# Kernel optimization log

Measured on AMD Instinct MI355X. Metric: run time of the kernel, lower is better.

## Reference

```python
import jax, jax.numpy as jnp
import numpy as np

B, T, D = 2, 2048, 1024
H, DH, CTX = 16, 64, 2048
EPS = 1e-6

def setup_inputs() -> dict:
    key = jax.random.key(0)
    ks = jax.random.split(key, 8)
    s = lambda d: 1.0 / np.sqrt(d)
    return {
        'x':       jax.random.normal(ks[0], (B, T, D), jnp.float32),
        'w_norm1': jnp.ones((D,), jnp.float32),
        'w_qkv':   jax.random.normal(ks[1], (3 * D, D), jnp.float32) * s(D),
        'w_proj':  jax.random.normal(ks[2], (D, D), jnp.float32) * s(D),
        'w_norm2': jnp.ones((D,), jnp.float32),
        'w_gate':  jax.random.normal(ks[3], (4 * D, D), jnp.float32) * s(D),
        'w_up':    jax.random.normal(ks[4], (4 * D, D), jnp.float32) * s(D),
        'w_down':  jax.random.normal(ks[5], (D, 4 * D), jnp.float32) * s(4 * D),
        'step':    0,
    }

def _rmsnorm(x, w):
    return x * jax.lax.rsqrt(jnp.mean(x * x, axis=-1, keepdims=True) + EPS) * w

def reference(x, w_norm1, w_qkv, w_proj, w_norm2, w_gate, w_up, w_down, step):
    # Prefill path (kv_cache is None, step == 0): full causal attention over T tokens.
    b, t, d = x.shape
    scale = 1.0 / np.sqrt(DH)
    h = _rmsnorm(x, w_norm1)
    qkv = (h @ w_qkv.T).reshape(b, t, 3, H, DH).transpose(2, 0, 3, 1, 4)  # [3,B,H,T,Dh]
    q, k, v = qkv[0], qkv[1], qkv[2]
    att = jnp.einsum('bhqd,bhkd->bhqk', q, k) * scale           # [B,H,T,T]
    causal = jnp.tril(jnp.ones((t, t), bool))
    att = jnp.where(causal, att, jnp.float32(-jnp.inf))
    att = jax.nn.softmax(att, axis=-1)
    out = jnp.einsum('bhqk,bhkd->bhqd', att, v)                 # [B,H,T,Dh]
    out = out.transpose(0, 2, 1, 3).reshape(b, t, d)
    x = x + out @ w_proj.T
    h2 = _rmsnorm(x, w_norm2)
    x = x + (jax.nn.silu(h2 @ w_gate.T) * (h2 @ w_up.T)) @ w_down.T
    # Append-only KV cache, zero-padded to ctx length as in the torch module.
    k_cache = jnp.zeros((b, H, CTX, DH), x.dtype).at[:, :, :t].set(k)
    v_cache = jnp.zeros((b, H, CTX, DH), x.dtype).at[:, :, :t].set(v)
    return (x, k_cache, v_cache)
```

## Files before the change

kernel.cpp:

```cpp
#include <hip/hip_runtime.h>
#include <hip/hip_bf16.h>
#include <cstdint>
#include <cstddef>


using bf16x8 = __attribute__((ext_vector_type(8))) __bf16;
using f32x4  = __attribute__((ext_vector_type(4))) float;

#define VMCNT(n) asm volatile("s_waitcnt vmcnt(" #n ")" ::: "memory")
#define LGKM0()  do { asm volatile("s_waitcnt lgkmcnt(0)" ::: "memory"); \
                      __builtin_amdgcn_sched_barrier(0); } while (0)
#define BARF()   do { asm volatile("" ::: "memory"); __builtin_amdgcn_s_barrier(); \
                      asm volatile("" ::: "memory"); } while (0)

__device__ __forceinline__ short f2b(float f) {
  uint32_t u = __builtin_bit_cast(uint32_t, f);
  uint32_t r = (u + 0x7FFFu + ((u >> 16) & 1u)) >> 16;
  return (short)r;
}
__device__ __forceinline__ float b2f(short s) {
  uint32_t u = ((uint32_t)(uint16_t)s) << 16;
  return __builtin_bit_cast(float, u);
}
__device__ __forceinline__ uint32_t pack2(float a, float b) {
  return (__builtin_bit_cast(uint32_t, a) >> 16) |
         (__builtin_bit_cast(uint32_t, b) & 0xFFFF0000u);
}

__device__ __forceinline__ void gload16(const short* g, short* l) {
  __builtin_amdgcn_global_load_lds(
      (const __attribute__((address_space(1))) void*)g,
      (__attribute__((address_space(3))) void*)l, 16, 0, 0);
}

template<int ROWS>
__device__ __forceinline__ void stage_swz(const short* __restrict__ g, int ldg,
                                          short* lds, int tid) {
#pragma unroll
  for (int jj = 0; jj < ROWS / 32; ++jj) {
    int row = jj * 32 + (tid >> 3);
    int seg = tid & 7;
    gload16(g + (size_t)row * ldg + ((seg ^ (row & 7)) << 3),
            lds + row * 64 + (seg << 3));
  }
}

__device__ __forceinline__ void stage_round512(const short* __restrict__ g, int ldg,
                                               short* lds, int tid, int rbase) {
  int row = rbase + (tid >> 3);
  int seg = tid & 7;
  gload16(g + (size_t)row * ldg + ((seg ^ (row & 7)) << 3),
          lds + row * 64 + (seg << 3));
}

__device__ __forceinline__ bf16x8 frag64(const short* lds, int row, int seg) {
  return *(const bf16x8*)(lds + row * 64 + ((seg ^ (row & 7)) << 3));
}

__device__ __forceinline__ f32x4 mma16(bf16x8 a, bf16x8 b, f32x4 c) {
  return __builtin_amdgcn_mfma_f32_16x16x32_bf16(a, b, c, 0, 0, 0);
}

__global__ void k_cvt_all(const float* __restrict__ wqkv, short* __restrict__ oqkv,
                          const float* __restrict__ wproj, short* __restrict__ oproj,
                          const float* __restrict__ wgate, short* __restrict__ ogate,
                          const float* __restrict__ wup, short* __restrict__ oup,
                          const float* __restrict__ wdown, short* __restrict__ odown) {
  int bid = blockIdx.x;
  const float* src;
  short* dst;
  int off;
  if (bid < 3072)       { src = wqkv;  dst = oqkv;  off = bid; }
  else if (bid < 4096)  { src = wproj; dst = oproj; off = bid - 3072; }
  else if (bid < 8192)  { src = wgate; dst = ogate; off = bid - 4096; }
  else if (bid < 12288) { src = wup;   dst = oup;   off = bid - 8192; }
  else                  { src = wdown; dst = odown; off = bid - 12288; }
  int i = off * 256 + threadIdx.x;
  float4 v = ((const float4*)src)[i];
  ((short4*)dst)[i] = make_short4(f2b(v.x), f2b(v.y), f2b(v.z), f2b(v.w));
}

__global__ void k_rms(const float* __restrict__ x, const float* __restrict__ w,
                      short* __restrict__ out) {
  int row = blockIdx.x;
  int tid = threadIdx.x;
  float4 v = *(const float4*)(x + (size_t)row * 1024 + tid * 4);
  float ss = v.x * v.x + v.y * v.y + v.z * v.z + v.w * v.w;
#pragma unroll
  for (int o = 1; o < 64; o <<= 1) ss += __shfl_xor(ss, o);
  __shared__ float sred[4];
  int wid = tid >> 6, lane = tid & 63;
  if (lane == 0) sred[wid] = ss;
  __syncthreads();
  float tot = sred[0] + sred[1] + sred[2] + sred[3];
  float r = rsqrtf(tot * (1.0f / 1024.0f) + 1e-6f);
  float4 wv = *(const float4*)(w + tid * 4);
  short4 o = make_short4(f2b(v.x * r * wv.x), f2b(v.y * r * wv.y),
                         f2b(v.z * r * wv.z), f2b(v.w * r * wv.w));
  *(short4*)(out + (size_t)row * 1024 + tid * 4) = o;
}

template<int MODE>
__global__ __launch_bounds__(512, 2) void k_gemm_big(
    const short* __restrict__ A, const short* __restrict__ Bw,
    int M, int N, int K, int gx,
    short* __restrict__ outb,
    short* __restrict__ q_b, short* __restrict__ k_b, short* __restrict__ vT_b,
    float* __restrict__ kc, float* __restrict__ vc) {
  __shared__ short As[2][256 * 64];
  __shared__ short Bs[2][256 * 64];
  int tid = threadIdx.x;
  int nwg = gridDim.x, bid = blockIdx.x;
  int swz = (bid & 7) * (nwg >> 3) + (bid >> 3);
  int bx = swz % gx, by = swz / gx;
  int m0 = by * 256, n0 = bx * 256;
  int w = tid >> 6, l = tid & 63;
  int wr = w >> 2, wc = w & 3;
  int lr = l & 15, lseg = l >> 4;
  f32x4 acc[2][2][4][2] = {};
  int nk = K >> 6;
  const short* Ab = A + (size_t)m0 * K;
  const short* Bb = Bw + (size_t)n0 * K;

  stage_round512(Ab, K, &As[0][0], tid, 0);
  stage_round512(Ab, K, &As[0][0], tid, 64);
  stage_round512(Ab, K, &As[0][0], tid, 128);
  stage_round512(Ab, K, &As[0][0], tid, 192);
  stage_round512(Bb, K, &Bs[0][0], tid, 0);
  stage_round512(Bb, K, &Bs[0][0], tid, 64);
  stage_round512(Bb, K, &Bs[0][0], tid, 128);
  stage_round512(Bb, K, &Bs[0][0], tid, 192);
  stage_round512(Ab + 64, K, &As[1][0], tid, 0);
  stage_round512(Ab + 64, K, &As[1][0], tid, 128);
  stage_round512(Ab + 64, K, &As[1][0], tid, 64);
  stage_round512(Ab + 64, K, &As[1][0], tid, 192);
  stage_round512(Bb + 64, K, &Bs[1][0], tid, 0);
  stage_round512(Bb + 64, K, &Bs[1][0], tid, 64);

  bf16x8 a0[4][2], a1[4][2], bq[2][2];
#pragma unroll 2
  for (int t = 0; t < nk; ++t) {
    short* Sa  = &As[t & 1][0];
    short* Sb  = &Bs[t & 1][0];
    short* Sb1 = &Bs[(t + 1) & 1][0];
    const short* Ag2 = Ab + (size_t)(t + 2) * 64;
    const short* Bg1 = Bb + (size_t)(t + 1) * 64;
    const short* Bg2 = Bb + (size_t)(t + 2) * 64;
    bool pf1 = (t + 1 < nk), pf2 = (t + 2 < nk);

    VMCNT(6);
    BARF();

#pragma unroll
    for (int i = 0; i < 4; ++i)
#pragma unroll
      for (int kk = 0; kk < 2; ++kk)
        a0[i][kk] = frag64(Sa, wr * 128 + i * 16 + lr, kk * 4 + lseg);
#pragma unroll
    for (int j = 0; j < 2; ++j)
#pragma unroll
      for (int kk = 0; kk < 2; ++kk)
        bq[j][kk] = frag64(Sb, wc * 64 + j * 16 + lr, kk * 4 + lseg);
    if (pf1) {
      stage_round512(Bg1, K, Sb1, tid, 128);
      stage_round512(Bg1, K, Sb1, tid, 192);
    }
    BARF();
    LGKM0();
    __builtin_amdgcn_s_setprio(1);
#pragma unroll
    for (int i = 0; i < 4; ++i)
#pragma unroll
      for (int j = 0; j < 2; ++j) {
        acc[0][0][i][j] = mma16(a0[i][0], bq[j][0], acc[0][0][i][j]);
        acc[0][0][i][j] = mma16(a0[i][1], bq[j][1], acc[0][0][i][j]);
      }
    __builtin_amdgcn_s_setprio(0);

#pragma unroll
    for (int i = 0; i < 4; ++i)
#pragma unroll
      for (int kk = 0; kk < 2; ++kk)
        a1[i][kk] = frag64(Sa, wr * 128 + 64 + i * 16 + lr, kk * 4 + lseg);
    if (pf2) {
      stage_round512(Ag2, K, Sa, tid, 0);
      stage_round512(Ag2, K, Sa, tid, 128);
    }
    BARF();
    LGKM0();
    __builtin_amdgcn_s_setprio(1);
#pragma unroll
    for (int i = 0; i < 4; ++i)
#pragma unroll
      for (int j = 0; j < 2; ++j) {
        acc[1][0][i][j] = mma16(a1[i][0], bq[j][0], acc[1][0][i][j]);
        acc[1][0][i][j] = mma16(a1[i][1], bq[j][1], acc[1][0][i][j]);
      }
    __builtin_amdgcn_s_setprio(0);

#pragma unroll
    for (int j = 0; j < 2; ++j)
#pragma unroll
      for (int kk = 0; kk < 2; ++kk)
        bq[j][kk] = frag64(Sb, wc * 64 + 32 + j * 16 + lr, kk * 4 + lseg);
    if (pf2) {
      stage_round512(Ag2, K, Sa, tid, 64);
      stage_round512(Ag2, K, Sa, tid, 192);
    }
    BARF();
    LGKM0();
    __builtin_amdgcn_s_setprio(1);
#pragma unroll
    for (int i = 0; i < 4; ++i)
#pragma unroll
      for (int j = 0; j < 2; ++j) {
        acc[0][1][i][j] = mma16(a0[i][0], bq[j][0], acc[0][1][i][j]);
        acc[0][1][i][j] = mma16(a0[i][1], bq[j][1], acc[0][1][i][j]);
      }
    __builtin_amdgcn_s_setprio(0);

    if (pf2) {
      stage_round512(Bg2, K, Sb, tid, 0);
      stage_round512(Bg2, K, Sb, tid, 64);
    }
    BARF();
    __builtin_amdgcn_s_setprio(1);
#pragma unroll
    for (int i = 0; i < 4; ++i)
#pragma unroll
      for (int j = 0; j < 2; ++j) {
        acc[1][1][i][j] = mma16(a1[i][0], bq[j][0], acc[1][1][i][j]);
        acc[1][1][i][j] = mma16(a1[i][1], bq[j][1], acc[1][1][i][j]);
      }
    __builtin_amdgcn_s_setprio(0);
  }

#pragma unroll
  for (int qm = 0; qm < 2; ++qm) {
#pragma unroll
    for (int qn = 0; qn < 2; ++qn) {
#pragma unroll
      for (int i = 0; i < 4; ++i) {
#pragma unroll
        for (int j = 0; j < 2; ++j) {
#pragma unroll
          for (int r = 0; r < 4; ++r) {
            int m = m0 + wr * 128 + qm * 64 + i * 16 + (l >> 4) * 4 + r;
            int n = n0 + wc * 64 + qn * 32 + j * 16 + lr;
            float f = acc[qm][qn][i][j][r];
            if (MODE == 1) {
              outb[(size_t)m * N + n] = f2b(f);
            } else if (MODE == 2) {
              float g = b2f(outb[(size_t)m * N + n]);
              float sg = g / (1.0f + __expf(-g));
              outb[(size_t)m * N + n] = f2b(sg * f);
            } else {
              int jj = n >> 10, hh = (n >> 6) & 15, dh = n & 63;
              int b_ = m >> 11, t = m & 2047;
              int bhh = b_ * 16 + hh;
              size_t idx = ((size_t)bhh * 2048 + t) * 64 + dh;
              if (jj == 0) {
                q_b[idx] = f2b(f);
              } else if (jj == 1) {
                k_b[idx] = f2b(f);
                kc[idx] = f;
              } else {
                vT_b[((size_t)bhh * 64 + dh) * 2048 + t] = f2b(f);
                vc[idx] = f;
              }
            }
          }
        }
      }
    }
  }
}

__global__ __launch_bounds__(256, 2) void k_gemm_skinny(
    const short* __restrict__ A, const short* __restrict__ Bw,
    int M, int N, int K, int gx,
    const float* __restrict__ res, float* __restrict__ outf) {
  __shared__ short As[3][128 * 64];
  __shared__ short Bs[3][64 * 64];
  int tid = threadIdx.x;
  int nwg = gridDim.x, bid = blockIdx.x;
  int swz = (bid & 7) * (nwg >> 3) + (bid >> 3);
  int bx = swz % gx, by = swz / gx;
  int m0 = by * 128, n0 = bx * 64;
  int w = tid >> 6, l = tid & 63;
  int wr = w >> 1, wc = w & 1;
  int lr = l & 15, lseg = l >> 4;
  f32x4 acc[4][2] = {};
  int nk = K >> 6;
  const short* Ab = A + (size_t)m0 * K;
  const short* Bb = Bw + (size_t)n0 * K;

  stage_swz<128>(Ab, K, &As[0][0], tid);
  stage_swz<64>(Bb, K, &Bs[0][0], tid);
  stage_swz<128>(Ab + 64, K, &As[1][0], tid);
  stage_swz<64>(Bb + 64, K, &Bs[1][0], tid);

#pragma unroll 1
  for (int u = 0; u < nk; ++u) {
    VMCNT(6);
    BARF();
    if (u + 2 < nk) {
      int sl = (u + 2) % 3;
      stage_swz<128>(Ab + (u + 2) * 64, K, &As[sl][0], tid);
      stage_swz<64>(Bb + (u + 2) * 64, K, &Bs[sl][0], tid);
    }
    const short* Asl = &As[u % 3][0];
    const short* Bsl = &Bs[u % 3][0];
    bf16x8 ar[4][2], br[2][2];
#pragma unroll
    for (int i = 0; i < 4; ++i)
#pragma unroll
      for (int kk = 0; kk < 2; ++kk)
        ar[i][kk] = frag64(Asl, wr * 64 + i * 16 + lr, kk * 4 + lseg);
#pragma unroll
    for (int j = 0; j < 2; ++j)
#pragma unroll
      for (int kk = 0; kk < 2; ++kk)
        br[j][kk] = frag64(Bsl, wc * 32 + j * 16 + lr, kk * 4 + lseg);
    LGKM0();
    __builtin_amdgcn_s_setprio(1);
#pragma unroll
    for (int i = 0; i < 4; ++i)
#pragma unroll
      for (int j = 0; j < 2; ++j) {
        acc[i][j] = mma16(ar[i][0], br[j][0], acc[i][j]);
        acc[i][j] = mma16(ar[i][1], br[j][1], acc[i][j]);
      }
    __builtin_amdgcn_s_setprio(0);
  }

#pragma unroll
  for (int i = 0; i < 4; ++i) {
#pragma unroll
    for (int j = 0; j < 2; ++j) {
#pragma unroll
      for (int r = 0; r < 4; ++r) {
        int m = m0 + wr * 64 + i * 16 + (l >> 4) * 4 + r;
        int n = n0 + wc * 32 + j * 16 + lr;
        outf[(size_t)m * N + n] = acc[i][j][r] + res[(size_t)m * N + n];
      }
    }
  }
}

template<int NC>
__device__ __forceinline__ void attn_tile(
    const short* __restrict__ Ksl, const short* __restrict__ Vsl,
    short* __restrict__ pw,
    const bf16x8 (&qf)[2][2], f32x4 (&acc)[2][4],
    float (&mrow)[2], float (&dden)[2],
    int kv0, int qb0, int qb1, bool band0, bool band1,
    int lr, int g) {
  bf16x8 kf[4][2], vb[2][4];
#pragma unroll
  for (int i = 0; i < 4; ++i)
#pragma unroll
    for (int kk = 0; kk < 2; ++kk)
      kf[i][kk] = frag64(Ksl, i * 16 + lr, kk * 4 + g);
#pragma unroll
  for (int kk = 0; kk < 2; ++kk)
#pragma unroll
    for (int jf = 0; jf < 4; ++jf)
      vb[kk][jf] = frag64(Vsl, jf * 16 + lr, kk * 4 + g);

  f32x4 st[NC][4];
#pragma unroll
  for (int c = 0; c < NC; ++c) {
    int cc = (NC == 2) ? c : 1;
#pragma unroll
    for (int i = 0; i < 4; ++i) {
      f32x4 z = {};
      z = mma16(kf[i][0], qf[cc][0], z);
      z = mma16(kf[i][1], qf[cc][1], z);
      st[c][i] = z;
    }
  }

  const float SC = 0.125f * 1.44269504f;
  float p[NC][16], pm[NC], corr[NC];
#pragma unroll
  for (int c = 0; c < NC; ++c) {
    int cc = (NC == 2) ? c : 1;
    bool band = (cc == 0) ? band0 : band1;
    int qgc = ((cc == 0) ? qb0 : qb1) + lr;
    float m_ = -INFINITY;
#pragma unroll
    for (int i = 0; i < 4; ++i)
#pragma unroll
      for (int r = 0; r < 4; ++r) {
        float v = st[c][i][r] * SC;
        if (band) {
          int key = kv0 + i * 16 + g * 4 + r;
          if (key > qgc) v = -INFINITY;
        }
        p[c][i * 4 + r] = v;
        m_ = fmaxf(m_, v);
      }
    pm[c] = m_;
  }
#pragma unroll
  for (int c = 0; c < NC; ++c) pm[c] = fmaxf(pm[c], __shfl_xor(pm[c], 16));
#pragma unroll
  for (int c = 0; c < NC; ++c) pm[c] = fmaxf(pm[c], __shfl_xor(pm[c], 32));
  float dsum[NC];
#pragma unroll
  for (int c = 0; c < NC; ++c) {
    int cc = (NC == 2) ? c : 1;
    float nm = fmaxf(mrow[cc], pm[c]);
    corr[c] = exp2f(mrow[cc] - nm);
    mrow[cc] = nm;
    float ds_ = 0.0f;
#pragma unroll
    for (int kx = 0; kx < 16; ++kx) {
      float pv = exp2f(p[c][kx] - nm);
      p[c][kx] = pv;
      ds_ += pv;
    }
    dsum[c] = ds_;
  }
#pragma unroll
  for (int c = 0; c < NC; ++c) dsum[c] += __shfl_xor(dsum[c], 16);
#pragma unroll
  for (int c = 0; c < NC; ++c) dsum[c] += __shfl_xor(dsum[c], 32);
#pragma unroll
  for (int c = 0; c < NC; ++c) {
    int cc = (NC == 2) ? c : 1;
    dden[cc] = dden[cc] * corr[c] + dsum[c];
  }

#pragma unroll
  for (int c = 0; c < NC; ++c) {
    int cc = (NC == 2) ? c : 1;
#pragma unroll
    for (int r = 0; r < 4; ++r) {
      float cr = __shfl(corr[c], g * 4 + r);
#pragma unroll
      for (int jf = 0; jf < 4; ++jf) acc[cc][jf][r] *= cr;
    }
    int prow = cc * 16 + lr;
#pragma unroll
    for (int i = 0; i < 4; ++i) {
      uint2 pk;
      pk.x = pack2(p[c][i * 4 + 0], p[c][i * 4 + 1]);
      pk.y = pack2(p[c][i * 4 + 2], p[c][i * 4 + 3]);
      int seg = (i * 2 + (g >> 1)) ^ (prow & 7);
      *(uint2*)(pw + prow * 64 + seg * 8 + (g & 1) * 4) = pk;
    }
  }

#pragma unroll
  for (int c = 0; c < NC; ++c) {
    int cc = (NC == 2) ? c : 1;
    int prow = cc * 16 + lr;
#pragma unroll
    for (int kk = 0; kk < 2; ++kk) {
      bf16x8 pa = *(const bf16x8*)(pw + prow * 64 + (((kk * 4 + g) ^ (prow & 7)) << 3));
#pragma unroll
      for (int jf = 0; jf < 4; ++jf)
        acc[cc][jf] = mma16(pa, vb[kk][jf], acc[cc][jf]);
    }
  }
}

__global__ __launch_bounds__(256, 2) void k_attn(const short* __restrict__ q_b,
                                                 const short* __restrict__ k_b,
                                                 const short* __restrict__ vT_b,
                                                 short* __restrict__ o_b) {
  __shared__ short Ks[3][64 * 64];
  __shared__ short VTs[3][64 * 64];
  __shared__ short Ps[4][32 * 64];
  int tid = threadIdx.x;
  int w = tid >> 6, l = tid & 63;
  int lr = l & 15, g = l >> 4;
  int ib = blockIdx.x, bh = blockIdx.y;
  int qlo = ib, qhi = 31 - ib;
  int qb0 = qlo * 64 + w * 16;
  int qb1 = qhi * 64 + w * 16;

  bf16x8 qf[2][2];
  const short* Qg = q_b + (size_t)bh * 2048 * 64;
#pragma unroll
  for (int kk = 0; kk < 2; ++kk) {
    qf[0][kk] = *(const bf16x8*)(Qg + (size_t)(qb0 + lr) * 64 + kk * 32 + g * 8);
    qf[1][kk] = *(const bf16x8*)(Qg + (size_t)(qb1 + lr) * 64 + kk * 32 + g * 8);
  }

  f32x4 acc[2][4] = {};
  float mrow[2] = {-INFINITY, -INFINITY};
  float dden[2] = {0.0f, 0.0f};
  int nt = qhi + 1;
  const short* Kg = k_b + (size_t)bh * 2048 * 64;
  const short* Vg = vT_b + (size_t)bh * 64 * 2048;
  short* pw = &Ps[w][0];

  stage_swz<64>(Kg, 64, &Ks[0][0], tid);
  stage_swz<64>(Vg, 2048, &VTs[0][0], tid);
  stage_swz<64>(Kg + 64 * 64, 64, &Ks[1][0], tid);
  stage_swz<64>(Vg + 64, 2048, &VTs[1][0], tid);

#pragma unroll 1
  for (int kt = 0; kt <= qlo; ++kt) {
    VMCNT(4);
    BARF();
    if (kt + 2 < nt) {
      int sl = (kt + 2) % 3;
      stage_swz<64>(Kg + (size_t)(kt + 2) * 64 * 64, 64, &Ks[sl][0], tid);
      stage_swz<64>(Vg + (kt + 2) * 64, 2048, &VTs[sl][0], tid);
    }
    int s = kt % 3;
    attn_tile<2>(&Ks[s][0], &VTs[s][0], pw, qf, acc, mrow, dden,
                 kt * 64, qb0, qb1, kt == qlo, false, lr, g);
  }
#pragma unroll 1
  for (int kt = qlo + 1; kt < nt; ++kt) {
    VMCNT(4);
    BARF();
    if (kt + 2 < nt) {
      int sl = (kt + 2) % 3;
      stage_swz<64>(Kg + (size_t)(kt + 2) * 64 * 64, 64, &Ks[sl][0], tid);
      stage_swz<64>(Vg + (kt + 2) * 64, 2048, &VTs[sl][0], tid);
    }
    int s = kt % 3;
    attn_tile<1>(&Ks[s][0], &VTs[s][0], pw, qf, acc, mrow, dden,
                 kt * 64, qb0, qb1, false, kt == qhi, lr, g);
  }

  int hh = bh & 15, b_ = bh >> 4;
#pragma unroll
  for (int c = 0; c < 2; ++c) {
    int qbc = (c == 0) ? qb0 : qb1;
#pragma unroll
    for (int r = 0; r < 4; ++r) {
      float dq = __shfl(dden[c], g * 4 + r);
      float inv = 1.0f / dq;
      int mg = qbc + g * 4 + r;
      size_t rowoff = ((size_t)b_ * 2048 + mg) * 1024 + hh * 64;
#pragma unroll
      for (int jf = 0; jf < 4; ++jf)
        o_b[rowoff + jf * 16 + lr] = f2b(acc[c][jf][r] * inv);
    }
  }
}

extern "C" void kernel_launch(void* const* d_in, const int* in_sizes, int n_in,
                              void* d_out, int out_size, void* d_ws, size_t ws_size,
                              hipStream_t stream) {
  const float* x     = (const float*)d_in[0];
  const float* wn1   = (const float*)d_in[1];
  const float* wqkv  = (const float*)d_in[2];
  const float* wproj = (const float*)d_in[3];
  const float* wn2   = (const float*)d_in[4];
  const float* wgate = (const float*)d_in[5];
  const float* wup   = (const float*)d_in[6];
  const float* wdown = (const float*)d_in[7];
  float* out = (float*)d_out;
  char* ws = (char*)d_ws;

  short* wqkv_b  = (short*)(ws + 0);
  short* wproj_b = (short*)(ws + 6291456);
  short* wgate_b = (short*)(ws + 8388608);
  short* wup_b   = (short*)(ws + 16777216);
  short* wdown_b = (short*)(ws + 25165824);
  short* h_b     = (short*)(ws + 33554432);
  short* q_b     = (short*)(ws + 41943040);
  short* k_b     = (short*)(ws + 50331648);
  short* vT_b    = (short*)(ws + 58720256);
  short* ao_b    = (short*)(ws + 67108864);
  short* act_b   = q_b;
  float* x1 = out;
  float* kc = out + 4194304;
  float* vc = out + 8388608;

  k_cvt_all<<<16384, 256, 0, stream>>>(wqkv, wqkv_b, wproj, wproj_b,
                                       wgate, wgate_b, wup, wup_b, wdown, wdown_b);

  k_rms<<<4096, 256, 0, stream>>>(x, wn1, h_b);

  k_gemm_big<3><<<192, 512, 0, stream>>>(h_b, wqkv_b, 4096, 3072, 1024, 12,
                                         nullptr, q_b, k_b, vT_b, kc, vc);

  k_attn<<<dim3(16, 32), 256, 0, stream>>>(q_b, k_b, vT_b, ao_b);

  k_gemm_skinny<<<512, 256, 0, stream>>>(ao_b, wproj_b, 4096, 1024, 1024, 16,
                                         x, x1);

  k_rms<<<4096, 256, 0, stream>>>(x1, wn2, h_b);

  k_gemm_big<1><<<256, 512, 0, stream>>>(h_b, wgate_b, 4096, 4096, 1024, 16,
                                         act_b, nullptr, nullptr, nullptr, nullptr, nullptr);
  k_gemm_big<2><<<256, 512, 0, stream>>>(h_b, wup_b, 4096, 4096, 1024, 16,
                                         act_b, nullptr, nullptr, nullptr, nullptr, nullptr);
  k_gemm_skinny<<<512, 256, 0, stream>>>(act_b, wdown_b, 4096, 1024, 4096, 16,
                                         x1, out);
}
```

Baseline: 320.8 us.

## Fuse gate and up GEMMs with SiLU into a single dual-accumulator kernel

Replaces the two separate gate/up GEMM launches, where the second reread the bf16 gate output to apply SiLU, with one kernel. That kernel stages the A tile once, multiplies it against both gate and up weight tiles, and applies silu(g)*u in the epilogue. This removes a full write and reread of the 4096x4096 intermediate and halves the loads of the A operand. The cost is a smaller N tile (128), doubled accumulator registers that may lower occupancy, and a new hand-scheduled pipeline.

Result: faster. 301.2 us (-6.1%).

```diff
diff --git a/kernel.cpp b/kernel.cpp
--- a/kernel.cpp
+++ b/kernel.cpp
@@ -250,10 +250,6 @@
             float f = acc[qm][qn][i][j][r];
             if (MODE == 1) {
               outb[(size_t)m * N + n] = f2b(f);
-            } else if (MODE == 2) {
-              float g = b2f(outb[(size_t)m * N + n]);
-              float sg = g / (1.0f + __expf(-g));
-              outb[(size_t)m * N + n] = f2b(sg * f);
             } else {
               int jj = n >> 10, hh = (n >> 6) & 15, dh = n & 63;
               int b_ = m >> 11, t = m & 2047;
@@ -270,6 +266,157 @@
               }
             }
           }
+        }
+      }
+    }
+  }
+}
+
+__global__ __launch_bounds__(512) void k_mlp(
+    const short* __restrict__ A, const short* __restrict__ Wg,
+    const short* __restrict__ Wu, short* __restrict__ outb) {
+  const int K = 1024, N = 4096, nk = 16;
+  __shared__ short As[2][256 * 64];
+  __shared__ short Bg[2][128 * 64];
+  __shared__ short Bu[2][128 * 64];
+  int tid = threadIdx.x;
+  int nwg = gridDim.x, bid = blockIdx.x;
+  int swz = (bid & 7) * (nwg >> 3) + (bid >> 3);
+  int bx = swz & 31, by = swz >> 5;
+  int m0 = by * 256, n0 = bx * 128;
+  int w = tid >> 6, l = tid & 63;
+  int wr = w >> 2, wc = w & 3;
+  int lr = l & 15, lseg = l >> 4;
+  f32x4 aG[2][4][2] = {}, aU[2][4][2] = {};
+  const short* Ab = A + (size_t)m0 * K;
+  const short* Gb = Wg + (size_t)n0 * K;
+  const short* Ub = Wu + (size_t)n0 * K;
+
+  stage_round512(Ab, K, &As[0][0], tid, 0);
+  stage_round512(Ab, K, &As[0][0], tid, 64);
+  stage_round512(Ab, K, &As[0][0], tid, 128);
+  stage_round512(Ab, K, &As[0][0], tid, 192);
+  stage_round512(Gb, K, &Bg[0][0], tid, 0);
+  stage_round512(Gb, K, &Bg[0][0], tid, 64);
+  stage_round512(Ub, K, &Bu[0][0], tid, 0);
+  stage_round512(Ub, K, &Bu[0][0], tid, 64);
+  stage_round512(Ab + 64, K, &As[1][0], tid, 0);
+  stage_round512(Ab + 64, K, &As[1][0], tid, 64);
+  stage_round512(Ab + 64, K, &As[1][0], tid, 128);
+  stage_round512(Ab + 64, K, &As[1][0], tid, 192);
+
+  bf16x8 a0[4][2], a1[4][2], bg[2][2], bu[2][2];
+#pragma unroll 2
+  for (int t = 0; t < nk; ++t) {
+    short* Sa  = &As[t & 1][0];
+    short* Sg  = &Bg[t & 1][0];
+    short* Su  = &Bu[t & 1][0];
+    short* SgN = &Bg[(t + 1) & 1][0];
+    short* SuN = &Bu[(t + 1) & 1][0];
+    const short* Ag2 = Ab + (size_t)(t + 2) * 64;
+    const short* Gg1 = Gb + (size_t)(t + 1) * 64;
+    const short* Ug1 = Ub + (size_t)(t + 1) * 64;
+    bool pf1 = (t + 1 < nk), pf2 = (t + 2 < nk);
+
+    VMCNT(4);
+    BARF();
+
+#pragma unroll
+    for (int i = 0; i < 4; ++i)
+#pragma unroll
+      for (int kk = 0; kk < 2; ++kk)
+        a0[i][kk] = frag64(Sa, wr * 128 + i * 16 + lr, kk * 4 + lseg);
+#pragma unroll
+    for (int j = 0; j < 2; ++j)
+#pragma unroll
+      for (int kk = 0; kk < 2; ++kk)
+        bg[j][kk] = frag64(Sg, wc * 32 + j * 16 + lr, kk * 4 + lseg);
+    if (pf1) {
+      stage_round512(Gg1, K, SgN, tid, 0);
+      stage_round512(Gg1, K, SgN, tid, 64);
+      stage_round512(Ug1, K, SuN, tid, 0);
+      stage_round512(Ug1, K, SuN, tid, 64);
+    }
+    BARF();
+    LGKM0();
+    __builtin_amdgcn_s_setprio(1);
+#pragma unroll
+    for (int i = 0; i < 4; ++i)
+#pragma unroll
+      for (int j = 0; j < 2; ++j) {
+        aG[0][i][j] = mma16(a0[i][0], bg[j][0], aG[0][i][j]);
+        aG[0][i][j] = mma16(a0[i][1], bg[j][1], aG[0][i][j]);
+      }
+    __builtin_amdgcn_s_setprio(0);
+
+#pragma unroll
+    for (int j = 0; j < 2; ++j)
+#pragma unroll
+      for (int kk = 0; kk < 2; ++kk)
+        bu[j][kk] = frag64(Su, wc * 32 + j * 16 + lr, kk * 4 + lseg);
+    if (pf2) {
+      stage_round512(Ag2, K, Sa, tid, 0);
+      stage_round512(Ag2, K, Sa, tid, 128);
+    }
+    BARF();
+    LGKM0();
+    __builtin_amdgcn_s_setprio(1);
+#pragma unroll
+    for (int i = 0; i < 4; ++i)
+#pragma unroll
+      for (int j = 0; j < 2; ++j) {
+        aU[0][i][j] = mma16(a0[i][0], bu[j][0], aU[0][i][j]);
+        aU[0][i][j] = mma16(a0[i][1], bu[j][1], aU[0][i][j]);
+      }
+    __builtin_amdgcn_s_setprio(0);
+
+#pragma unroll
+    for (int i = 0; i < 4; ++i)
+#pragma unroll
+      for (int kk = 0; kk < 2; ++kk)
+        a1[i][kk] = frag64(Sa, wr * 128 + 64 + i * 16 + lr, kk * 4 + lseg);
+    BARF();
+    LGKM0();
+    __builtin_amdgcn_s_setprio(1);
+#pragma unroll
+    for (int i = 0; i < 4; ++i)
+#pragma unroll
+      for (int j = 0; j < 2; ++j) {
+        aG[1][i][j] = mma16(a1[i][0], bg[j][0], aG[1][i][j]);
+        aG[1][i][j] = mma16(a1[i][1], bg[j][1], aG[1][i][j]);
+      }
+    __builtin_amdgcn_s_setprio(0);
+
+    if (pf2) {
+      stage_round512(Ag2, K, Sa, tid, 64);
+      stage_round512(Ag2, K, Sa, tid, 192);
+    }
+    BARF();
+    __builtin_amdgcn_s_setprio(1);
+#pragma unroll
+    for (int i = 0; i < 4; ++i)
+#pragma unroll
+      for (int j = 0; j < 2; ++j) {
+        aU[1][i][j] = mma16(a1[i][0], bu[j][0], aU[1][i][j]);
+        aU[1][i][j] = mma16(a1[i][1], bu[j][1], aU[1][i][j]);
+      }
+    __builtin_amdgcn_s_setprio(0);
+  }
+
+#pragma unroll
+  for (int qm = 0; qm < 2; ++qm) {
+#pragma unroll
+    for (int i = 0; i < 4; ++i) {
+#pragma unroll
+      for (int j = 0; j < 2; ++j) {
+#pragma unroll
+        for (int r = 0; r < 4; ++r) {
+          int m = m0 + wr * 128 + qm * 64 + i * 16 + (l >> 4) * 4 + r;
+          int n = n0 + wc * 32 + j * 16 + lr;
+          float g = aG[qm][i][j][r];
+          float u = aU[qm][i][j][r];
+          float s = g / (1.0f + __expf(-g));
+          outb[(size_t)m * N + n] = f2b(s * u);
         }
       }
     }
@@ -591,10 +738,8 @@
 
   k_rms<<<4096, 256, 0, stream>>>(x1, wn2, h_b);
 
-  k_gemm_big<1><<<256, 512, 0, stream>>>(h_b, wgate_b, 4096, 4096, 1024, 16,
-                                         act_b, nullptr, nullptr, nullptr, nullptr, nullptr);
-  k_gemm_big<2><<<256, 512, 0, stream>>>(h_b, wup_b, 4096, 4096, 1024, 16,
-                                         act_b, nullptr, nullptr, nullptr, nullptr, nullptr);
+  k_mlp<<<512, 512, 0, stream>>>(h_b, wgate_b, wup_b, act_b);
+
   k_gemm_skinny<<<512, 256, 0, stream>>>(act_b, wdown_b, 4096, 1024, 4096, 16,
                                          x1, out);
 }
```
